# Performance work log

Measured on AMD Instinct MI355X. Metric: run time of the kernel, lower is better.

Reference implementation:

```python
import jax, jax.numpy as jnp
import numpy as np

B, CIN, H, W = 16, 1, 256, 256
COUT = 1
L = 4          # nr_fno_layers
CH = 64        # fno_layer_size
M1 = M2 = 16   # fno_modes
PAD = 8
GROUPS = 4
EPS = 1e-5


def gelu(x):
    return jax.nn.gelu(x, approximate=False)  # torch F.gelu default (erf)


def conv1x1(x, w, b):
    # x: [B,C,H,W], w: [O,C], b: [O]
    return jnp.einsum('bchw,oc->bohw', x, w) + b[None, :, None, None]


def group_norm(x, gamma, beta):
    b, c, h, w = x.shape
    xg = x.reshape(b, GROUPS, c // GROUPS, h, w)
    mu = xg.mean(axis=(2, 3, 4), keepdims=True)
    var = xg.var(axis=(2, 3, 4), keepdims=True)
    xn = ((xg - mu) / jnp.sqrt(var + EPS)).reshape(b, c, h, w)
    return xn * gamma[None, :, None, None] + beta[None, :, None, None]


def spectral_conv(x, w1, w2):
    # x: [B,C,Hp,Wp]; w1,w2: [C,C,M1,M2,2] real/imag
    b, c, hp, wp = x.shape
    xf = jnp.fft.rfft2(x)                      # [B,C,Hp,Wp//2+1] complex
    cw1 = w1[..., 0] + 1j * w1[..., 1]
    cw2 = w2[..., 0] + 1j * w2[..., 1]
    lo = jnp.einsum('bixy,ioxy->boxy', xf[:, :, :M1, :M2], cw1)
    hi = jnp.einsum('bixy,ioxy->boxy', xf[:, :, -M1:, :M2], cw2)
    out_ft = jnp.zeros((b, c, hp, wp // 2 + 1), dtype=jnp.complex64)
    out_ft = out_ft.at[:, :, :M1, :M2].set(lo).at[:, :, -M1:, :M2].set(hi)
    return jnp.fft.irfft2(out_ft, s=(hp, wp))


def setup_inputs() -> dict:
    key = jax.random.key(0)
    ks = jax.random.split(key, 12)
    scale = 1.0 / (CH * CH)
    return {
        'x': jax.random.normal(ks[0], (B, CIN, H, W), jnp.float32),
        'lift_w': jax.random.normal(ks[1], (CH, CIN), jnp.float32) * (1.0 / np.sqrt(CIN)),
        'lift_b': jnp.zeros((CH,), jnp.float32),
        'sp_w1': scale * jax.random.uniform(ks[2], (L, CH, CH, M1, M2, 2), jnp.float32),
        'sp_w2': scale * jax.random.uniform(ks[3], (L, CH, CH, M1, M2, 2), jnp.float32),
        'conv_w': jax.random.normal(ks[4], (L, CH, CH), jnp.float32) * (1.0 / np.sqrt(CH)),
        'conv_b': jnp.zeros((L, CH), jnp.float32),
        'gn_g': jnp.ones((L, CH), jnp.float32),
        'gn_b': jnp.zeros((L, CH), jnp.float32),
        'dec_w1': jax.random.normal(ks[5], (CH, CH), jnp.float32) * (1.0 / np.sqrt(CH)),
        'dec_b1': jnp.zeros((CH,), jnp.float32),
        'dec_w2': jax.random.normal(ks[6], (COUT, CH), jnp.float32) * (1.0 / np.sqrt(CH)),
        'dec_b2': jnp.zeros((COUT,), jnp.float32),
    }


def reference(x, lift_w, lift_b, sp_w1, sp_w2, conv_w, conv_b, gn_g, gn_b,
              dec_w1, dec_b1, dec_w2, dec_b2):
    # lift (Conv2dFCLayer, identity activation, bias frozen at 0)
    h = conv1x1(x, lift_w, lift_b)
    # F.pad(x, (0, PAD, 0, PAD)): pad right of W and bottom of H
    h = jnp.pad(h, ((0, 0), (0, 0), (0, PAD), (0, PAD)))
    for k in range(L):
        sp = spectral_conv(h, sp_w1[k], sp_w2[k])
        y = group_norm(sp, gn_g[k], gn_b[k]) + conv1x1(h, conv_w[k], conv_b[k])
        h = gelu(y) if k < L - 1 else y
    # unpad
    h = h[..., :-PAD, :-PAD]
    # decoder projection: conv1x1 -> gelu -> conv1x1
    h = conv1x1(h, dec_w1, dec_b1)
    h = gelu(h)
    h = conv1x1(h, dec_w2, dec_b2)
    return h
```

## Files before the change

### kernel.cpp

```cpp
#include <hip/hip_runtime.h>
#include <hip/hip_bf16.h>
#include <math.h>

#define PH   264
#define NPIX (PH*PH)
#define NBAT 16
#define NIMG (NBAT*64)
#define NLAY 4

typedef unsigned short ushort_t;
typedef unsigned int   uint_t;
typedef _Float16       half_t;
typedef __attribute__((ext_vector_type(8))) short short8;
typedef __attribute__((ext_vector_type(4))) float float4v;

__device__ __forceinline__ float blo(uint_t u){ union{uint_t u; float f;} v; v.u = u << 16;        return v.f; }
__device__ __forceinline__ float bhi(uint_t u){ union{uint_t u; float f;} v; v.u = u & 0xffff0000u; return v.f; }
__device__ __forceinline__ float b2f(ushort_t s){ union{uint_t u; float f;} v; v.u = ((uint_t)s) << 16; return v.f; }
__device__ __forceinline__ ushort_t f2b(float f){
  __hip_bfloat16 h = __float2bfloat16(f);
  union{__hip_bfloat16 h; ushort_t s;} v; v.h = h; return v.s;
}
__device__ __forceinline__ float gelu_f(float v){
  float x2 = v*v;
  float u  = v*fmaf(0.044715f, x2, 1.0f);
  float e  = __builtin_amdgcn_exp2f(-2.3022082f*u);
  return v*__builtin_amdgcn_rcpf(1.0f + e);
}

__global__ __launch_bounds__(256) void k_tables(float* __restrict__ tFT, float* __restrict__ tCT,
                                                float* __restrict__ tST,
                                                ushort_t* __restrict__ TWh, ushort_t* __restrict__ TWl,
                                                const float* __restrict__ cw, ushort_t* __restrict__ cwB){
  int idx = blockIdx.x*256 + threadIdx.x;
  const double W0 = 6.283185307179586 / 264.0;
  if (idx < 8448){
    int y = idx >> 5, kk = idx & 31, k = kk >> 1;
    int ph = (k*y) % 264;
    float ang = (float)(W0 * ph), s, c;
    sincosf(ang, &s, &c);
    tFT[idx] = (kk & 1) ? -s : c;
  } else if (idx < 16896){
    int d = idx - 8448;
    int x = d >> 5, kxi = d & 31;
    int kxe = (kxi < 16) ? kxi : kxi - 32;
    int ph = ((kxe*x) % 264 + 264) % 264;
    float ang = (float)(W0 * ph), s, c;
    sincosf(ang, &s, &c);
    tCT[d] = c; tST[d] = s;
  } else if (idx < 16896 + 8704){
    int d = idx - 16896;
    int y = d >> 5, kk = d & 31;
    float v = 0.f;
    if (y < 264){
      if (kk == 0) v = 0.5f;
      else if (kk > 1){
        int j = kk >> 1;
        int ph = (j*y) % 264;
        float ang = (float)(W0 * ph), s, c;
        sincosf(ang, &s, &c);
        v = (kk & 1) ? -s : c;
      }
    }
    ushort_t hi = f2b(v);
    TWh[d] = hi;
    TWl[d] = f2b(v - b2f(hi));
  } else if (idx < 25600 + 16384){
    int d = idx - 25600;
    cwB[d] = f2b(cw[d]);
  }
}

__global__ __launch_bounds__(256) void k_fwd_y0(const float* __restrict__ xin, const float* __restrict__ lw,
                                                const float* __restrict__ lb, const float* __restrict__ tFT,
                                                half_t* __restrict__ tmp){
  int t = threadIdx.x;
  int row = blockIdx.x*4 + (t>>6);
  int c = t & 63;
  int b = row / 264, x = row - b*264;
  float acc[32];
#pragma unroll
  for (int j=0;j<32;++j) acc[j]=0.f;
  if (x < 256){
    float lwc = lw[c], lbc = lb[c];
    const float* xp = xin + ((size_t)(b*256+x))*256;
    for (int y=0; y<256; ++y){
      float h = lwc*xp[y] + lbc;
      const float* fr = tFT + y*32;
#pragma unroll
      for (int j=0;j<32;++j) acc[j] += h*fr[j];
    }
  }
  half_t* op = tmp + (((size_t)row)*32)*64 + c;
#pragma unroll
  for (int j=0;j<32;++j) op[(size_t)j*64] = (half_t)acc[j];
}

__global__ __launch_bounds__(256) void k_fwd_y(const ushort_t* __restrict__ H, const float* __restrict__ tFT,
                                               half_t* __restrict__ tmp){
  int t = threadIdx.x;
  int row = blockIdx.x*4 + (t>>6);
  int c = t & 63;
  int b = row / 264, x = row - b*264;
  const ushort_t* hp = H + ((size_t)b*NPIX + (size_t)x*PH)*64 + c;
  float acc[32];
#pragma unroll
  for (int j=0;j<32;++j) acc[j]=0.f;
  for (int y=0; y<PH; ++y){
    float h = b2f(hp[(size_t)y*64]);
    const float* fr = tFT + y*32;
#pragma unroll
    for (int j=0;j<32;++j) acc[j] += h*fr[j];
  }
  half_t* op = tmp + (((size_t)row)*32)*64 + c;
#pragma unroll
  for (int j=0;j<32;++j) op[(size_t)j*64] = (half_t)acc[j];
}

__global__ __launch_bounds__(256) void k_fwd_x(const half_t* __restrict__ tmp, const float* __restrict__ tCT,
                                               const float* __restrict__ tST, float* __restrict__ Xf){
  int t = threadIdx.x, b = blockIdx.y;
  int m = blockIdx.x*4 + (t>>6);
  int c = t & 63;
  int kxi = m >> 4, ky = m & 15;
  float xr=0.f, xi=0.f;
  const half_t* base = tmp + ((size_t)b*264*32 + 2*ky)*64 + c;
  for (int x=0; x<PH; ++x){
    float tr = (float)base[(size_t)x*32*64];
    float ti = (float)base[(size_t)x*32*64 + 64];
    float cc = tCT[x*32+kxi], ss = tST[x*32+kxi];
    xr += tr*cc + ti*ss;
    xi += ti*cc - tr*ss;
  }
  ((float2*)Xf)[(size_t)(b*64+c)*512 + m] = make_float2(xr, xi);
}

__global__ __launch_bounds__(512) void k_mix(const float* __restrict__ Xf, const float* __restrict__ w1,
                                             const float* __restrict__ w2, float* __restrict__ oft){
  int m = threadIdx.x;
  int o = blockIdx.x;
  int b0 = blockIdx.y*4;
  const float2* X = (const float2*)Xf;
  const float2* W = (const float2*)((m < 256) ? w1 : w2);
  int mm = m & 255;
  float2 acc[4];
#pragma unroll
  for (int b=0;b<4;++b) acc[b] = make_float2(0.f,0.f);
  for (int i=0;i<64;++i){
    float2 w = W[(size_t)(i*64+o)*256 + mm];
#pragma unroll
    for (int b=0;b<4;++b){
      float2 x = X[((size_t)((b0+b)*64+i)*512) + m];
      acc[b].x += x.x*w.x - x.y*w.y;
      acc[b].y += x.x*w.y + x.y*w.x;
    }
  }
  float2* O = (float2*)oft;
#pragma unroll
  for (int b=0;b<4;++b) O[((size_t)((b0+b)*64+o)*512) + m] = acc[b];
}

__global__ __launch_bounds__(256) void k_stats_spec(const float* __restrict__ oft, float2* __restrict__ stats){
  __shared__ float sq[256], s1s[256];
  int bg = blockIdx.x, t = threadIdx.x;
  int b = bg >> 2, g = bg & 3;
  const float2* O = (const float2*)oft;
  float q = 0.f, s1 = 0.f;
  for (int c16=0; c16<16; ++c16){
    const float2* Op = O + (size_t)(b*64 + g*16 + c16)*512;
    for (int m=t; m<512; m+=256){
      if (m & 15){ float2 v = Op[m]; q += 2.f*(v.x*v.x + v.y*v.y); }
    }
  }
  {
    int c16 = t >> 4, j = t & 15;
    const float2* Op = O + (size_t)(b*64 + g*16 + c16)*512;
    if (j == 0){
      float2 a0 = Op[0];
      s1 = a0.x;
      q += a0.x*a0.x;
      float2 h16 = Op[16*16];
      q += 0.5f*(h16.x*h16.x + h16.y*h16.y);
    } else {
      float2 a = Op[j*16];
      float2 bb = Op[(32-j)*16];
      float rr = a.x + bb.x, ii = a.y - bb.y;
      q += 0.5f*(rr*rr + ii*ii);
    }
  }
  sq[t] = q; s1s[t] = s1; __syncthreads();
  for (int st_=128; st_>0; st_>>=1){
    if (t < st_){ sq[t] += sq[t+st_]; s1s[t] += s1s[t+st_]; }
    __syncthreads();
  }
  if (t == 0){
    const float invN = 1.0f/1115136.0f;
    float mu  = s1s[0]*invN;
    float ssq = sq[0]*(1.0f/69696.0f);
    float var = fmaxf(ssq*invN - mu*mu, 0.f);
    stats[bg] = make_float2(mu, 1.0f/sqrtf(var + 1e-5f));
  }
}

__global__ __launch_bounds__(256) void k_inv_x(const float* __restrict__ oft, const float* __restrict__ tCT,
                                               const float* __restrict__ tST, ushort_t* __restrict__ zB,
                                               const float2* __restrict__ stats, const float* __restrict__ gg){
  __shared__ float sof[1024];
  int t = threadIdx.x, img = blockIdx.x;
  int b = img >> 6, c = img & 63;
  const float* op = oft + (size_t)img*1024;
  for (int d=t; d<1024; d+=256) sof[d] = op[d];
  __syncthreads();
  float al = stats[b*4 + (c>>4)].y * gg[c] * (2.0f/69696.0f);
  for (int x=t; x<264; x+=256){
    float zr[16], zi[16];
#pragma unroll
    for (int k=0;k<16;++k){ zr[k]=0.f; zi[k]=0.f; }
    for (int kxi=0; kxi<32; ++kxi){
      float cc = tCT[x*32+kxi], ss = tST[x*32+kxi];
#pragma unroll
      for (int ky=0; ky<16; ++ky){
        float orr = sof[(kxi*16+ky)*2], oii = sof[(kxi*16+ky)*2 + 1];
        zr[ky] += orr*cc - oii*ss;
        zi[ky] += oii*cc + orr*ss;
      }
    }
    uint_t wh[16], wl[16];
#pragma unroll
    for (int k=0;k<16;++k){
      float a = zr[k]*al, bb2 = zi[k]*al;
      ushort_t ah = f2b(a),  bh = f2b(bb2);
      ushort_t alo = f2b(a - b2f(ah)), blo_ = f2b(bb2 - b2f(bh));
      wh[k] = (uint_t)ah | ((uint_t)bh << 16);
      wl[k] = (uint_t)alo | ((uint_t)blo_ << 16);
    }
    uint4* dst = (uint4*)(zB + ((size_t)((size_t)(b*264 + x)*64 + c))*64);
#pragma unroll
    for (int q=0;q<4;++q) dst[q]   = ((uint4*)wh)[q];
#pragma unroll
    for (int q=0;q<4;++q) dst[4+q] = ((uint4*)wl)[q];
  }
}

__global__ __launch_bounds__(512, 4) void k_fused2(ushort_t* __restrict__ H,
                                                const ushort_t* __restrict__ zB,
                                                const ushort_t* __restrict__ cwB,
                                                const float* __restrict__ cb,
                                                const float* __restrict__ gg, const float* __restrict__ gb,
                                                const float2* __restrict__ stats,
                                                const ushort_t* __restrict__ TWh, const ushort_t* __restrict__ TWl,
                                                const float* __restrict__ xin, const float* __restrict__ lw,
                                                const float* __restrict__ lb,
                                                int do_gelu, int lay0){
  __shared__ short smem[9216];
  __shared__ float lwL[64], lbL[64];
  short* zBs = smem;
  short* cws = smem + 4608;
  int t = threadIdx.x, b = blockIdx.y, x = blockIdx.x;
  int w = t >> 6, lane = t & 63;
  int quad = lane >> 4, lcol = lane & 15;

  {
    int row = t >> 3, q = t & 7;
    const uint4* zsrc = (const uint4*)(zB + ((size_t)(b*264 + x))*64*64);
    *(uint4*)&zBs[row*72 + q*8] = zsrc[t];
    *(uint4*)&cws[row*72 + q*8] = ((const uint4*)cwB)[t];
  }
  if (t < 64){ lwL[t] = lw[t]; lbL[t] = lb[t]; }
  __syncthreads();

  float4v acc[3][4];
#pragma unroll
  for (int si=0;si<3;++si)
#pragma unroll
    for (int n=0;n<4;++n) acc[si][n] = (float4v){0.f,0.f,0.f,0.f};

#pragma unroll
  for (int si=0;si<3;++si){
    int mt = w + 8*si;
    if (mt > 16) break;
    int pxl = mt*16 + lcol;
    union{uint4 u; short8 s;} a0, a1;
    a0.u = make_uint4(0,0,0,0); a1.u = make_uint4(0,0,0,0);
    if (lay0){
      bool in = (x < 256) && (pxl < 256);
      float xv = in ? xin[((size_t)(b*256+x))*256 + pxl] : 0.f;
      uint_t wa[8];
#pragma unroll
      for (int j=0;j<4;++j){
        int ch = quad*8 + 2*j;
        float v0 = in ? (lwL[ch  ]*xv + lbL[ch  ]) : 0.f;
        float v1 = in ? (lwL[ch+1]*xv + lbL[ch+1]) : 0.f;
        wa[j] = (uint_t)f2b(v0) | ((uint_t)f2b(v1) << 16);
        float v2 = in ? (lwL[ch+32]*xv + lbL[ch+32]) : 0.f;
        float v3 = in ? (lwL[ch+33]*xv + lbL[ch+33]) : 0.f;
        wa[4+j] = (uint_t)f2b(v2) | ((uint_t)f2b(v3) << 16);
      }
      a0.u = make_uint4(wa[0], wa[1], wa[2], wa[3]);
      a1.u = make_uint4(wa[4], wa[5], wa[6], wa[7]);
    } else if (pxl < PH){
      const ushort_t* hp = H + ((size_t)b*NPIX + (size_t)x*PH + pxl)*64 + quad*8;
      a0.u = *(const uint4*)hp;
      a1.u = *(const uint4*)(hp + 32);
    }
    short8 Th = *(const short8*)(TWh + pxl*32 + quad*8);
    short8 Tl = *(const short8*)(TWl + pxl*32 + quad*8);
#pragma unroll
    for (int n=0;n<4;++n){
      float4v a = acc[si][n];
      short8 Bc0 = *(const short8*)&cws[(n*16+lcol)*72 + quad*8];
      short8 Bc1 = *(const short8*)&cws[(n*16+lcol)*72 + 32 + quad*8];
      a = __builtin_amdgcn_mfma_f32_16x16x32_bf16(a0.s, Bc0, a, 0, 0, 0);
      a = __builtin_amdgcn_mfma_f32_16x16x32_bf16(a1.s, Bc1, a, 0, 0, 0);
      short8 Bzh = *(const short8*)&zBs[(n*16+lcol)*72 + quad*8];
      short8 Bzl = *(const short8*)&zBs[(n*16+lcol)*72 + 32 + quad*8];
      a = __builtin_amdgcn_mfma_f32_16x16x32_bf16(Th, Bzh, a, 0, 0, 0);
      a = __builtin_amdgcn_mfma_f32_16x16x32_bf16(Th, Bzl, a, 0, 0, 0);
      a = __builtin_amdgcn_mfma_f32_16x16x32_bf16(Tl, Bzh, a, 0, 0, 0);
      acc[si][n] = a;
    }
  }

  __syncthreads();

  float beta[4];
#pragma unroll
  for (int n=0;n<4;++n){
    int o = n*16 + lcol;
    float2 st = stats[b*4 + n];
    beta[n] = gb[o] - st.x*st.y*gg[o] + cb[o];
  }
  short* ob = smem + w*1152;
#pragma unroll
  for (int si=0;si<3;++si){
    int mt = w + 8*si;
    if (mt > 16) break;
#pragma unroll
    for (int reg=0; reg<4; ++reg){
      int prow = quad*4 + reg;
#pragma unroll
      for (int n=0;n<4;++n){
        float v = acc[si][n][reg] + beta[n];
        if (do_gelu) v = gelu_f(v);
        ob[prow*72 + n*16 + lcol] = (short)f2b(v);
      }
    }
    asm volatile("s_waitcnt lgkmcnt(0)" ::: "memory");
#pragma unroll
    for (int p=0;p<2;++p){
      int prow2 = p*8 + (lane>>3);
      int c0 = (lane&7)*8;
      int pxl2 = mt*16 + prow2;
      if (pxl2 < PH){
        uint4 u = *(const uint4*)&ob[prow2*72 + c0];
        *(uint4*)(H + ((size_t)b*NPIX + (size_t)x*PH + pxl2)*64 + c0) = u;
      }
    }
    asm volatile("" ::: "memory");
  }
}

__global__ __launch_bounds__(256) void k_dec(const ushort_t* __restrict__ H, const float* __restrict__ w1,
                                             const float* __restrict__ b1, const float* __restrict__ w2,
                                             const float* __restrict__ b2, float* __restrict__ out){
  __shared__ short w1h[64*72], w1l[64*72];
  __shared__ float w2L[64], b1L[64];
  int t = threadIdx.x, x = blockIdx.x, b = blockIdx.y;
  for (int d=t; d<4096; d+=256){
    int o = d>>6, c = d&63;
    float v = w1[o*64+c];
    ushort_t hi = f2b(v);
    w1h[o*72+c] = (short)hi;
    w1l[o*72+c] = (short)f2b(v - b2f(hi));
  }
  if (t < 64){ w2L[t] = w2[t]; b1L[t] = b1[t]; }
  __syncthreads();

  int w = t >> 6, lane = t & 63;
  int quad = lane >> 4, lcol = lane & 15;
  float bias2 = b2[0];

#pragma unroll
  for (int i=0;i<4;++i){
    int mt = w*4 + i;
    int py = mt*16 + lcol;
    const ushort_t* hp = H + ((size_t)b*NPIX + (size_t)x*PH + py)*64 + quad*8;
    union{uint4 u; short8 s;} a0, a1;
    a0.u = *(const uint4*)hp;
    a1.u = *(const uint4*)(hp + 32);

    float4v acc[4];
#pragma unroll
    for (int n=0;n<4;++n) acc[n] = (float4v){0.f,0.f,0.f,0.f};
#pragma unroll
    for (int n=0;n<4;++n){
      float4v a = acc[n];
      short8 Bh0 = *(const short8*)&w1h[(n*16+lcol)*72 + quad*8];
      short8 Bh1 = *(const short8*)&w1h[(n*16+lcol)*72 + 32 + quad*8];
      short8 Bl0 = *(const short8*)&w1l[(n*16+lcol)*72 + quad*8];
      short8 Bl1 = *(const short8*)&w1l[(n*16+lcol)*72 + 32 + quad*8];
      a = __builtin_amdgcn_mfma_f32_16x16x32_bf16(a0.s, Bh0, a, 0, 0, 0);
      a = __builtin_amdgcn_mfma_f32_16x16x32_bf16(a1.s, Bh1, a, 0, 0, 0);
      a = __builtin_amdgcn_mfma_f32_16x16x32_bf16(a0.s, Bl0, a, 0, 0, 0);
      a = __builtin_amdgcn_mfma_f32_16x16x32_bf16(a1.s, Bl1, a, 0, 0, 0);
      acc[n] = a;
    }

    float s0=0.f, s1=0.f, s2=0.f, s3=0.f;
#pragma unroll
    for (int n=0;n<4;++n){
      int o = n*16 + lcol;
      float wv = w2L[o];
      float bb = b1L[o];
      s0 += wv*gelu_f(acc[n][0] + bb);
      s1 += wv*gelu_f(acc[n][1] + bb);
      s2 += wv*gelu_f(acc[n][2] + bb);
      s3 += wv*gelu_f(acc[n][3] + bb);
    }
#pragma unroll
    for (int m=1;m<16;m<<=1){
      s0 += __shfl_xor(s0, m, 64);
      s1 += __shfl_xor(s1, m, 64);
      s2 += __shfl_xor(s2, m, 64);
      s3 += __shfl_xor(s3, m, 64);
    }
    if (lcol < 4){
      float v = (lcol==0) ? s0 : (lcol==1) ? s1 : (lcol==2) ? s2 : s3;
      out[((size_t)b*256 + x)*256 + mt*16 + quad*4 + lcol] = v + bias2;
    }
  }
}

extern "C" void kernel_launch(void* const* d_in, const int* in_sizes, int n_in,
                              void* d_out, int out_size, void* d_ws, size_t ws_size,
                              hipStream_t stream){
  const float* x    = (const float*)d_in[0];
  const float* liw  = (const float*)d_in[1];
  const float* lib  = (const float*)d_in[2];
  const float* w1   = (const float*)d_in[3];
  const float* w2   = (const float*)d_in[4];
  const float* cw   = (const float*)d_in[5];
  const float* cb   = (const float*)d_in[6];
  const float* gg   = (const float*)d_in[7];
  const float* gb   = (const float*)d_in[8];
  const float* dw1  = (const float*)d_in[9];
  const float* db1  = (const float*)d_in[10];
  const float* dw2  = (const float*)d_in[11];
  const float* db2  = (const float*)d_in[12];
  float* out = (float*)d_out;

  char* p = (char*)d_ws;
  ushort_t* H = (ushort_t*)p; p += (size_t)NBAT*NPIX*64*2;
  half_t* tmp = (half_t*)p; p += (size_t)NBAT*264*32*64*2;
  ushort_t* zB = (ushort_t*)p; p += (size_t)NBAT*264*64*64*2;
  float* Xf   = (float*)p; p += (size_t)NIMG*512*2*4;
  float* oft  = (float*)p; p += (size_t)NIMG*512*2*4;
  float* tFT  = (float*)p; p += 8448*4;
  float* tCT  = (float*)p; p += 8448*4;
  float* tST  = (float*)p; p += 8448*4;
  ushort_t* TWh = (ushort_t*)p; p += 8704*2;
  ushort_t* TWl = (ushort_t*)p; p += 8704*2;
  ushort_t* cwB = (ushort_t*)p; p += 16384*2;
  float2* stats = (float2*)p; p += 64*8;

  k_tables<<<164, 256, 0, stream>>>(tFT, tCT, tST, TWh, TWl, cw, cwB);

  for (int k=0;k<NLAY;++k){
    if (k == 0)
      k_fwd_y0<<<1056, 256, 0, stream>>>(x, liw, lib, tFT, tmp);
    else
      k_fwd_y<<<1056, 256, 0, stream>>>(H, tFT, tmp);
    k_fwd_x<<<dim3(128,16), 256, 0, stream>>>(tmp, tCT, tST, Xf);
    k_mix<<<dim3(64,4), 512, 0, stream>>>(Xf, w1 + (size_t)k*2097152, w2 + (size_t)k*2097152, oft);
    k_stats_spec<<<64, 256, 0, stream>>>(oft, stats);
    k_inv_x<<<1024, 256, 0, stream>>>(oft, tCT, tST, zB, stats, gg + (size_t)k*64);
    k_fused2<<<dim3(264,16), 512, 0, stream>>>(H, zB, cwB + (size_t)k*4096, cb + (size_t)k*64,
                                               gg + (size_t)k*64, gb + (size_t)k*64, stats, TWh, TWl,
                                               x, liw, lib, (k<3)?1:0, (k==0)?1:0);
  }
  k_dec<<<dim3(256,16), 256, 0, stream>>>(H, dw1, db1, dw2, db2, out);
}
```

Before: 1.329 ms.

## Split k_mix into smaller blocks and peel tail pixel tile in fused kernel

k_mix now runs 256-thread blocks with two batches per block instead of 512 threads with four, giving four times as many blocks to fill the GPU. In k_fused2, the third pixel-tile iteration, which only warp 0 used for the 8-pixel tail, is replaced by a peeled tile handled by four warps, each computing one 16-channel output column. This drops the acc array from 3x4 to 2x4 plus one accumulator, reducing register pressure and removing bounds checks from the main loop. In exchange, k_mix reloads each weight twice as often across blocks, and the tail writes are scalar bf16 stores.

```diff
diff --git a/kernel.cpp b/kernel.cpp
--- a/kernel.cpp
+++ b/kernel.cpp
@@ -135,21 +135,20 @@
   ((float2*)Xf)[(size_t)(b*64+c)*512 + m] = make_float2(xr, xi);
 }
 
-__global__ __launch_bounds__(512) void k_mix(const float* __restrict__ Xf, const float* __restrict__ w1,
+__global__ __launch_bounds__(256) void k_mix(const float* __restrict__ Xf, const float* __restrict__ w1,
                                              const float* __restrict__ w2, float* __restrict__ oft){
-  int m = threadIdx.x;
-  int o = blockIdx.x;
-  int b0 = blockIdx.y*4;
+  int mm = threadIdx.x;
+  int o = blockIdx.x >> 1, half = blockIdx.x & 1;
+  int m = half*256 + mm;
+  int b0 = blockIdx.y*2;
   const float2* X = (const float2*)Xf;
-  const float2* W = (const float2*)((m < 256) ? w1 : w2);
-  int mm = m & 255;
-  float2 acc[4];
-#pragma unroll
-  for (int b=0;b<4;++b) acc[b] = make_float2(0.f,0.f);
+  const float2* W = (const float2*)(half ? w2 : w1);
+  float2 acc[2];
+  acc[0] = make_float2(0.f,0.f); acc[1] = make_float2(0.f,0.f);
   for (int i=0;i<64;++i){
     float2 w = W[(size_t)(i*64+o)*256 + mm];
 #pragma unroll
-    for (int b=0;b<4;++b){
+    for (int b=0;b<2;++b){
       float2 x = X[((size_t)((b0+b)*64+i)*512) + m];
       acc[b].x += x.x*w.x - x.y*w.y;
       acc[b].y += x.x*w.y + x.y*w.x;
@@ -157,7 +156,7 @@
   }
   float2* O = (float2*)oft;
 #pragma unroll
-  for (int b=0;b<4;++b) O[((size_t)((b0+b)*64+o)*512) + m] = acc[b];
+  for (int b=0;b<2;++b) O[((size_t)((b0+b)*64+o)*512) + m] = acc[b];
 }
 
 __global__ __launch_bounds__(256) void k_stats_spec(const float* __restrict__ oft, float2* __restrict__ stats){
@@ -269,21 +268,20 @@
   if (t < 64){ lwL[t] = lw[t]; lbL[t] = lb[t]; }
   __syncthreads();
 
-  float4v acc[3][4];
-#pragma unroll
-  for (int si=0;si<3;++si)
+  float4v acc[2][4];
+#pragma unroll
+  for (int si=0;si<2;++si)
 #pragma unroll
     for (int n=0;n<4;++n) acc[si][n] = (float4v){0.f,0.f,0.f,0.f};
-
-#pragma unroll
-  for (int si=0;si<3;++si){
+  float4v acc16 = (float4v){0.f,0.f,0.f,0.f};
+
+#pragma unroll
+  for (int si=0;si<2;++si){
     int mt = w + 8*si;
-    if (mt > 16) break;
     int pxl = mt*16 + lcol;
     union{uint4 u; short8 s;} a0, a1;
-    a0.u = make_uint4(0,0,0,0); a1.u = make_uint4(0,0,0,0);
     if (lay0){
-      bool in = (x < 256) && (pxl < 256);
+      bool in = (x < 256);
       float xv = in ? xin[((size_t)(b*256+x))*256 + pxl] : 0.f;
       uint_t wa[8];
 #pragma unroll
@@ -298,7 +296,7 @@
       }
       a0.u = make_uint4(wa[0], wa[1], wa[2], wa[3]);
       a1.u = make_uint4(wa[4], wa[5], wa[6], wa[7]);
-    } else if (pxl < PH){
+    } else {
       const ushort_t* hp = H + ((size_t)b*NPIX + (size_t)x*PH + pxl)*64 + quad*8;
       a0.u = *(const uint4*)hp;
       a1.u = *(const uint4*)(hp + 32);
@@ -321,6 +319,29 @@
     }
   }
 
+  if (w < 4){
+    int pxl = 256 + lcol;
+    union{uint4 u; short8 s;} a0, a1;
+    a0.u = make_uint4(0,0,0,0); a1.u = make_uint4(0,0,0,0);
+    if (!lay0 && pxl < PH){
+      const ushort_t* hp = H + ((size_t)b*NPIX + (size_t)x*PH + pxl)*64 + quad*8;
+      a0.u = *(const uint4*)hp;
+      a1.u = *(const uint4*)(hp + 32);
+    }
+    short8 Th = *(const short8*)(TWh + pxl*32 + quad*8);
+    short8 Tl = *(const short8*)(TWl + pxl*32 + quad*8);
+    int n = w;
+    short8 Bc0 = *(const short8*)&cws[(n*16+lcol)*72 + quad*8];
+    short8 Bc1 = *(const short8*)&cws[(n*16+lcol)*72 + 32 + quad*8];
+    acc16 = __builtin_amdgcn_mfma_f32_16x16x32_bf16(a0.s, Bc0, acc16, 0, 0, 0);
+    acc16 = __builtin_amdgcn_mfma_f32_16x16x32_bf16(a1.s, Bc1, acc16, 0, 0, 0);
+    short8 Bzh = *(const short8*)&zBs[(n*16+lcol)*72 + quad*8];
+    short8 Bzl = *(const short8*)&zBs[(n*16+lcol)*72 + 32 + quad*8];
+    acc16 = __builtin_amdgcn_mfma_f32_16x16x32_bf16(Th, Bzh, acc16, 0, 0, 0);
+    acc16 = __builtin_amdgcn_mfma_f32_16x16x32_bf16(Th, Bzl, acc16, 0, 0, 0);
+    acc16 = __builtin_amdgcn_mfma_f32_16x16x32_bf16(Tl, Bzh, acc16, 0, 0, 0);
+  }
+
   __syncthreads();
 
   float beta[4];
@@ -332,9 +353,8 @@
   }
   short* ob = smem + w*1152;
 #pragma unroll
-  for (int si=0;si<3;++si){
+  for (int si=0;si<2;++si){
     int mt = w + 8*si;
-    if (mt > 16) break;
 #pragma unroll
     for (int reg=0; reg<4; ++reg){
       int prow = quad*4 + reg;
@@ -351,12 +371,24 @@
       int prow2 = p*8 + (lane>>3);
       int c0 = (lane&7)*8;
       int pxl2 = mt*16 + prow2;
-      if (pxl2 < PH){
-        uint4 u = *(const uint4*)&ob[prow2*72 + c0];
-        *(uint4*)(H + ((size_t)b*NPIX + (size_t)x*PH + pxl2)*64 + c0) = u;
+      uint4 u = *(const uint4*)&ob[prow2*72 + c0];
+      *(uint4*)(H + ((size_t)b*NPIX + (size_t)x*PH + pxl2)*64 + c0) = u;
+    }
+    asm volatile("" ::: "memory");
+  }
+  if (w < 4){
+    int o = w*16 + lcol;
+    float2 st = stats[b*4 + w];
+    float beta16 = gb[o] - st.x*st.y*gg[o] + cb[o];
+#pragma unroll
+    for (int reg=0; reg<4; ++reg){
+      int pxl = 256 + quad*4 + reg;
+      if (pxl < PH){
+        float v = acc16[reg] + beta16;
+        if (do_gelu) v = gelu_f(v);
+        H[((size_t)b*NPIX + (size_t)x*PH + pxl)*64 + o] = f2b(v);
       }
     }
-    asm volatile("" ::: "memory");
   }
 }
 
@@ -471,7 +503,7 @@
     else
       k_fwd_y<<<1056, 256, 0, stream>>>(H, tFT, tmp);
     k_fwd_x<<<dim3(128,16), 256, 0, stream>>>(tmp, tCT, tST, Xf);
-    k_mix<<<dim3(64,4), 512, 0, stream>>>(Xf, w1 + (size_t)k*2097152, w2 + (size_t)k*2097152, oft);
+    k_mix<<<dim3(128,8), 256, 0, stream>>>(Xf, w1 + (size_t)k*2097152, w2 + (size_t)k*2097152, oft);
     k_stats_spec<<<64, 256, 0, stream>>>(oft, stats);
     k_inv_x<<<1024, 256, 0, stream>>>(oft, tCT, tST, zB, stats, gg + (size_t)k*64);
     k_fused2<<<dim3(264,16), 512, 0, stream>>>(H, zB, cwB + (size_t)k*4096, cb + (size_t)k*64,
```

After: 1.304 ms. Within noise of the previous version (-1.9%).
